# Optimization experiments

Measured on AMD Instinct MI355X. Metric: run time of the kernel, lower is better.

## Reference

```python
import jax, jax.numpy as jnp
import numpy as np

B, E, P, L, D = 16, 2048, 16384, 5, 64  # batch, num_edges, num node-pairs, max_path_distance, edge_dim
EPS = 1e-9


def setup_inputs() -> dict:
    key = jax.random.key(0)
    k1, k2, k3 = jax.random.split(key, 3)
    edge_embedding = jax.random.normal(k1, (B, E, D), dtype=jnp.float32)
    # -1 marks padding (unused path slots), valid entries in [0, E)
    edge_paths = jax.random.randint(k2, (B, P, L), -1, E, dtype=jnp.int64)
    edge_vector = jax.random.normal(k3, (L, D), dtype=jnp.float32)
    return {"edge_embedding": edge_embedding, "edge_paths": edge_paths, "edge_vector": edge_vector}


def reference(edge_embedding, edge_paths, edge_vector):
    # edge_embedding: (B, E, D); edge_paths: (B, P, L) int with -1 padding; edge_vector: (L, D)
    edge_mask = edge_paths == -1                                     # (B, P, L)
    clamped = jnp.clip(edge_paths, 0, None)
    # batched gather: out[b, p, l, :] = edge_embedding[b, clamped[b, p, l], :]
    gathered = jax.vmap(lambda emb, idx: emb[idx])(edge_embedding, clamped)  # (B, P, L, D)
    gathered = jnp.where(edge_mask[..., None], jnp.zeros((), gathered.dtype), gathered)
    path_lengths = (~edge_mask).sum(axis=-1).astype(edge_embedding.dtype) + EPS  # (B, P)
    enc = jnp.einsum('beld,ld->be', gathered, edge_vector)           # (B, P)
    return enc / path_lengths
```

## Files before the change

### kernel.cpp

```cpp
#include <hip/hip_runtime.h>
#include <hip/hip_bf16.h>

#define B 16
#define E 2048
#define P 16384
#define L 5
#define D 64
#define EPS 1e-9f

__global__ void edge_proj_kernel(const float* __restrict__ emb,
                                 const float* __restrict__ ev,
                                 float* __restrict__ proj) {
    __shared__ float sev[L * D];
    for (int i = threadIdx.x; i < L * D; i += blockDim.x) sev[i] = ev[i];
    __syncthreads();

    int idx = blockIdx.x * blockDim.x + threadIdx.x;
    if (idx >= B * E) return;

    const float4* row = (const float4*)(emb + (size_t)idx * D);
    const float4* w4  = (const float4*)sev;

    float acc[L];
#pragma unroll
    for (int l = 0; l < L; ++l) acc[l] = 0.f;

#pragma unroll
    for (int c = 0; c < D / 4; ++c) {
        float4 v = row[c];
#pragma unroll
        for (int l = 0; l < L; ++l) {
            float4 w = w4[l * (D / 4) + c];
            acc[l] += v.x * w.x + v.y * w.y + v.z * w.z + v.w * w.w;
        }
    }

    float* p = proj + (size_t)idx * L;
#pragma unroll
    for (int l = 0; l < L; ++l) p[l] = acc[l];
}

__global__ void edge_gather_kernel(const int* __restrict__ paths,
                                   const float* __restrict__ proj,
                                   float* __restrict__ out) {
    int idx = blockIdx.x * blockDim.x + threadIdx.x;
    if (idx >= B * P) return;

    int b = idx >> 14;
    const float* pb = proj + (size_t)b * E * L;
    const int* pp = paths + (size_t)idx * L;

    float sum = 0.f;
    int cnt = 0;
#pragma unroll
    for (int l = 0; l < L; ++l) {
        int e = pp[l];
        bool valid = (e >= 0);
        int ec = valid ? e : 0;
        float v = pb[ec * L + l];
        sum += valid ? v : 0.f;
        cnt += valid ? 1 : 0;
    }
    out[idx] = sum / ((float)cnt + EPS);
}

extern "C" void kernel_launch(void* const* d_in, const int* in_sizes, int n_in,
                              void* d_out, int out_size, void* d_ws, size_t ws_size,
                              hipStream_t stream) {
    const float* emb   = (const float*)d_in[0];
    const int*   paths = (const int*)d_in[1];
    const float* ev    = (const float*)d_in[2];
    float* out  = (float*)d_out;
    float* proj = (float*)d_ws;

    edge_proj_kernel<<<(B * E + 63) / 64, 64, 0, stream>>>(emb, ev, proj);
    edge_gather_kernel<<<(B * P + 255) / 256, 256, 0, stream>>>(paths, proj, out);
}
```

Baseline: 72.74 us.

## Split projection rows across lane pairs and stage per-batch projections in LDS

The projection kernel now uses two threads per edge row, each covering half of D, and combines the partial dot products with a lane shuffle. Blocks grow to 256 threads, which doubles parallelism. The gather kernel now stages the whole per-batch projection table (E*L floats, 40KB) in shared memory, and each block handles 1024 paths of a single batch. Random gathers are therefore served from LDS instead of global/L2. The trade-off is a 40KB table copy per block and lower occupancy from the large shared allocation.

```diff
diff --git a/kernel.cpp b/kernel.cpp
--- a/kernel.cpp
+++ b/kernel.cpp
@@ -8,60 +8,72 @@
 #define D 64
 #define EPS 1e-9f
 
-__global__ void edge_proj_kernel(const float* __restrict__ emb,
-                                 const float* __restrict__ ev,
-                                 float* __restrict__ proj) {
+__global__ __launch_bounds__(256) void edge_proj_kernel(
+    const float* __restrict__ emb, const float* __restrict__ ev,
+    float* __restrict__ proj) {
     __shared__ float sev[L * D];
-    for (int i = threadIdx.x; i < L * D; i += blockDim.x) sev[i] = ev[i];
+    for (int i = threadIdx.x; i < L * D; i += 256) sev[i] = ev[i];
     __syncthreads();
 
-    int idx = blockIdx.x * blockDim.x + threadIdx.x;
-    if (idx >= B * E) return;
+    int gid  = blockIdx.x * 256 + threadIdx.x;
+    int row  = gid >> 1;
+    int half = gid & 1;
 
-    const float4* row = (const float4*)(emb + (size_t)idx * D);
+    const float4* src = (const float4*)(emb + (size_t)row * D + half * 32);
     const float4* w4  = (const float4*)sev;
 
-    float acc[L];
+    float acc[L] = {0.f, 0.f, 0.f, 0.f, 0.f};
 #pragma unroll
-    for (int l = 0; l < L; ++l) acc[l] = 0.f;
-
-#pragma unroll
-    for (int c = 0; c < D / 4; ++c) {
-        float4 v = row[c];
+    for (int c = 0; c < 8; ++c) {
+        float4 v = src[c];
 #pragma unroll
         for (int l = 0; l < L; ++l) {
-            float4 w = w4[l * (D / 4) + c];
+            float4 w = w4[l * 16 + half * 8 + c];
             acc[l] += v.x * w.x + v.y * w.y + v.z * w.z + v.w * w.w;
         }
     }
+#pragma unroll
+    for (int l = 0; l < L; ++l) acc[l] += __shfl_xor(acc[l], 1);
 
-    float* p = proj + (size_t)idx * L;
+    if (half == 0) {
+        float* p = proj + (size_t)row * L;
 #pragma unroll
-    for (int l = 0; l < L; ++l) p[l] = acc[l];
+        for (int l = 0; l < L; ++l) p[l] = acc[l];
+    }
 }
 
-__global__ void edge_gather_kernel(const int* __restrict__ paths,
-                                   const float* __restrict__ proj,
-                                   float* __restrict__ out) {
-    int idx = blockIdx.x * blockDim.x + threadIdx.x;
-    if (idx >= B * P) return;
+__global__ __launch_bounds__(256) void edge_gather_kernel(
+    const int* __restrict__ paths, const float* __restrict__ proj,
+    float* __restrict__ out) {
+    __shared__ float sproj[E * L];
+    int b = blockIdx.x & 15;
+    int g = blockIdx.x >> 4;
 
-    int b = idx >> 14;
-    const float* pb = proj + (size_t)b * E * L;
-    const int* pp = paths + (size_t)idx * L;
+    const float4* src = (const float4*)(proj + (size_t)b * E * L);
+    float4* dst = (float4*)sproj;
+#pragma unroll
+    for (int i = 0; i < (E * L) / 4 / 256; ++i)
+        dst[threadIdx.x + i * 256] = src[threadIdx.x + i * 256];
+    __syncthreads();
 
-    float sum = 0.f;
-    int cnt = 0;
+    int pbase = g * (P / 16);
 #pragma unroll
-    for (int l = 0; l < L; ++l) {
-        int e = pp[l];
-        bool valid = (e >= 0);
-        int ec = valid ? e : 0;
-        float v = pb[ec * L + l];
-        sum += valid ? v : 0.f;
-        cnt += valid ? 1 : 0;
+    for (int k = 0; k < 4; ++k) {
+        int p = pbase + k * 256 + threadIdx.x;
+        const int* pp = paths + ((size_t)b * P + p) * L;
+        float sum = 0.f;
+        int cnt = 0;
+#pragma unroll
+        for (int l = 0; l < L; ++l) {
+            int e = pp[l];
+            bool valid = (e >= 0);
+            int ec = valid ? e : 0;
+            float v = sproj[ec * L + l];
+            sum += valid ? v : 0.f;
+            cnt += valid ? 1 : 0;
+        }
+        out[(size_t)b * P + p] = sum / ((float)cnt + EPS);
     }
-    out[idx] = sum / ((float)cnt + EPS);
 }
 
 extern "C" void kernel_launch(void* const* d_in, const int* in_sizes, int n_in,
@@ -73,6 +85,6 @@
     float* out  = (float*)d_out;
     float* proj = (float*)d_ws;
 
-    edge_proj_kernel<<<(B * E + 63) / 64, 64, 0, stream>>>(emb, ev, proj);
-    edge_gather_kernel<<<(B * P + 255) / 256, 256, 0, stream>>>(paths, proj, out);
+    edge_proj_kernel<<<(2 * B * E) / 256, 256, 0, stream>>>(emb, ev, proj);
+    edge_gather_kernel<<<16 * B, 256, 0, stream>>>(paths, proj, out);
 }
```

New measurement: 68.47 us. 1.06x faster.
